# Performance work log

Hardware: AMD Instinct MI355X
Metric: run time of the kernel (lower is better)

Reference implementation:

```python
import jax, jax.numpy as jnp
import numpy as np

B, C, N, K, COUT = 4, 64, 8192, 16, 64
EPS = 1e-5  # BatchNorm1d default eps


def setup_inputs() -> dict:
    key = jax.random.key(0)
    k1, k2, k3 = jax.random.split(key, 3)
    x = jax.random.normal(k1, (B, C, N), dtype=jnp.float32)
    coords = jax.random.normal(k2, (B, 3, N), dtype=jnp.float32)
    # Linear(2C -> COUT) params
    W = jax.random.normal(k3, (2 * C, COUT), dtype=jnp.float32) * (1.0 / np.sqrt(2 * C))
    b = jnp.zeros((COUT,), dtype=jnp.float32)
    # BatchNorm1d affine params (train-mode batch stats, as in torch default)
    gamma = jnp.ones((COUT,), dtype=jnp.float32)
    beta = jnp.zeros((COUT,), dtype=jnp.float32)
    return {"x": x, "coords": coords, "W": W, "b": b, "gamma": gamma, "beta": beta}


def reference(x, coords, W, b, gamma, beta):
    k = min(K, max(N - 1, 1))
    # --- kNN in coordinate space (squared distances give same ordering as cdist) ---
    ct = jnp.swapaxes(coords, 1, 2)                      # (B, N, 3)
    sq = jnp.sum(ct * ct, axis=-1)                       # (B, N)
    d2 = sq[:, :, None] + sq[:, None, :] - 2.0 * jnp.einsum('bnd,bmd->bnm', ct, ct)
    _, idx = jax.lax.top_k(-d2, k + 1)                   # smallest k+1 distances
    idx = idx[:, :, 1:]                                  # drop self -> (B, N, k)
    # --- gather neighbor features ---
    xt = jnp.swapaxes(x, 1, 2)                           # (B, N, C)
    nb = jax.vmap(lambda f, i: f[i])(xt, idx)            # (B, N, k, C)
    center = jnp.broadcast_to(xt[:, :, None, :], nb.shape)
    edge = jnp.concatenate([center, nb - center], axis=-1)  # (B, N, k, 2C)
    # --- edge MLP: Linear -> BatchNorm1d (batch stats) -> ReLU ---
    h = jnp.einsum('bnkc,cd->bnkd', edge, W) + b         # (B, N, k, COUT)
    mean = jnp.mean(h, axis=(0, 1, 2))
    var = jnp.var(h, axis=(0, 1, 2))
    h = (h - mean) * jax.lax.rsqrt(var + EPS) * gamma + beta
    h = jax.nn.relu(h)
    # --- max-pool over k neighbors ---
    out = jnp.max(h, axis=2)                             # (B, N, COUT)
    return jnp.swapaxes(out, 1, 2)                       # (B, COUT, N)
```

## Files before the change

### kernel.cpp

```cpp
#include <hip/hip_runtime.h>


#define Bn 4
#define Cn 64
#define Nn 8192
#define Kn 16
#define NSL 8

typedef unsigned long long ull;

__global__ __launch_bounds__(256) void transpose_kernel(const float* __restrict__ x,
                                                        const float* __restrict__ coords,
                                                        float* __restrict__ xt,
                                                        float4* __restrict__ cpack) {
  __shared__ float tile[64][65];
  int bid = blockIdx.x;
  int b = bid >> 7;
  int n0 = (bid & 127) << 6;
  int tx = threadIdx.x & 63;
  int ty = threadIdx.x >> 6;
  for (int c = ty; c < 64; c += 4)
    tile[tx][c] = x[((size_t)b * 64 + c) * Nn + n0 + tx];
  if (ty == 0) {
    int n = n0 + tx;
    const float* cb = coords + (size_t)b * 3 * Nn;
    float cx = cb[n], cy = cb[Nn + n], cz = cb[2 * Nn + n];
    float cs = __fadd_rn(__fadd_rn(__fmul_rn(cx, cx), __fmul_rn(cy, cy)),
                         __fmul_rn(cz, cz));
    cpack[(size_t)b * Nn + n] = make_float4(cx, cy, cz, cs);
  }
  __syncthreads();
  for (int r = ty; r < 64; r += 4)
    xt[((size_t)b * Nn + n0 + r) * 64 + tx] = tile[r][tx];
}


#define RMAX(kv) do {                                         \
    ull _kk = (kv);                                           \
    _Pragma("unroll")                                         \
    for (int _u = 0; _u < 16; ++_u)                           \
      ad[_u] = (ad[_u] == thr) ? _kk : ad[_u];                \
    ull _t0 = ad[0] > ad[1] ? ad[0] : ad[1];                  \
    ull _t1 = ad[2] > ad[3] ? ad[2] : ad[3];                  \
    ull _t2 = ad[4] > ad[5] ? ad[4] : ad[5];                  \
    ull _t3 = ad[6] > ad[7] ? ad[6] : ad[7];                  \
    ull _t4 = ad[8] > ad[9] ? ad[8] : ad[9];                  \
    ull _t5 = ad[10] > ad[11] ? ad[10] : ad[11];              \
    ull _t6 = ad[12] > ad[13] ? ad[12] : ad[13];              \
    ull _t7 = ad[14] > ad[15] ? ad[14] : ad[15];              \
    ull _u0 = _t0 > _t1 ? _t0 : _t1;                          \
    ull _u1 = _t2 > _t3 ? _t2 : _t3;                          \
    ull _u2 = _t4 > _t5 ? _t4 : _t5;                          \
    ull _u3 = _t6 > _t7 ? _t6 : _t7;                          \
    ull _v0 = _u0 > _u1 ? _u0 : _u1;                          \
    ull _v1 = _u2 > _u3 ? _u2 : _u3;                          \
    thr = _v0 > _v1 ? _v0 : _v1;                              \
  } while (0)

__global__ __launch_bounds__(512) void knn_kernel(const float4* __restrict__ cpack,
                                                  int* __restrict__ knn) {
  __shared__ __align__(16) ull mk[(NSL - 1) * 16 * 64];
  float4* stage = (float4*)mk;
  __shared__ unsigned sthr[64];

  int bid = blockIdx.x;
  int b = bid >> 7;
  int q0 = (bid & 127) << 6;
  int tid = threadIdx.x;
  int q = tid & 63;
  int s = tid >> 6;
  int qg = q0 + q;

  const float4* cp = cpack + (size_t)b * Nn;
  float4 qc = cp[qg];
  float qs = qc.w;
  float qx2 = 2.f * qc.x, qy2 = 2.f * qc.y, qz2 = 2.f * qc.z;

  if (tid < 64) sthr[tid] = 0xFFFFFFFFu;

  ull ad[16];
#pragma unroll
  for (int i = 0; i < 16; ++i) ad[i] = 0xFFFFFFFF00000000ull | (unsigned)i;
  ull thr = 0xFFFFFFFF0000000Full;
  unsigned thr_hi = 0xFFFFFFFFu;

  for (int t = 0; t < Nn / 512; ++t) {
    __syncthreads();
    stage[tid] = cp[t * 512 + tid];
    __syncthreads();
#pragma unroll
    for (int half = 0; half < 2; ++half) {
      int loc = half * 256 + s * 32;
      int base = t * 512 + loc;
      unsigned sh = sthr[q];
      thr_hi = sh < thr_hi ? sh : thr_hi;
      unsigned mask = 0;
#pragma unroll 8
      for (int j = 0; j < 32; ++j) {
        float4 c4 = stage[loc + j];
        float dot2 = __fadd_rn(__fadd_rn(__fmul_rn(qx2, c4.x), __fmul_rn(qy2, c4.y)),
                               __fmul_rn(qz2, c4.z));
        float d2 = __fsub_rn(__fadd_rn(qs, c4.w), dot2);
        mask |= (__float_as_uint(d2) <= thr_hi) ? (1u << j) : 0u;
      }
      unsigned sj = (unsigned)(qg - base);
      if (sj < 32u) mask &= ~(1u << sj);
      while (__any(mask)) {
        if (mask) {
          int j = __ffs(mask) - 1;
          mask &= (mask - 1);
          float4 c4 = stage[loc + j];
          float dot2 = __fadd_rn(__fadd_rn(__fmul_rn(qx2, c4.x), __fmul_rn(qy2, c4.y)),
                                 __fmul_rn(qz2, c4.z));
          float d2 = __fsub_rn(__fadd_rn(qs, c4.w), dot2);
          ull key = ((ull)__float_as_uint(d2) << 32) | (unsigned)(base + j);
          if (key < thr) RMAX(key);
        }
      }
      unsigned lh = (unsigned)(thr >> 32);
      thr_hi = lh < thr_hi ? lh : thr_hi;
      atomicMin(&sthr[q], lh);
    }
  }

  __syncthreads();
  if (s > 0) {
#pragma unroll
    for (int i = 0; i < 16; ++i) mk[(((s - 1) << 4) + i) * 64 + q] = ad[i];
  }
  __syncthreads();
  if (s == 0) {
    for (int t = 0; t < (NSL - 1) * 16; ++t) {
      ull kk = mk[t * 64 + q];
      if (kk < thr) RMAX(kk);
    }
    int* op = knn + (size_t)(b * Nn + qg) * 16;
#pragma unroll
    for (int i = 0; i < 16; ++i) op[i] = (int)(ad[i] & 0xFFFFFFFFull);
  }
}

__global__ __launch_bounds__(256) void edge_kernel(
    const float* __restrict__ xt, const int* __restrict__ knn,
    const float* __restrict__ W, const float* __restrict__ bias,
    float* __restrict__ mnb, float* __restrict__ mxb,
    float* __restrict__ ps1, float* __restrict__ ps2) {
  __shared__ float dlds[4][16][64];
  __shared__ float clds[4][64];
  __shared__ float r1[4][64], r2[4][64];

  int tid = threadIdx.x;
  int l = tid & 63;
  int w = tid >> 6;

  float w1[64], w2[64];
#pragma unroll
  for (int c = 0; c < 64; ++c) {
    w1[c] = W[c * 64 + l];
    w2[c] = W[(64 + c) * 64 + l];
  }
  float bl = bias[l];
  float s1 = 0.f, s2 = 0.f;

  int wid = blockIdx.x * 4 + w;
  int nw = gridDim.x * 4;
  for (int p = wid; p < Bn * Nn; p += nw) {
    int bb = p >> 13;
    const float* xb = xt + (size_t)bb * Nn * 64;
    float ctr = xt[(size_t)p * 64 + l];
    clds[w][l] = ctr;
    const int* ip = knn + (size_t)p * 16;
#pragma unroll
    for (int j = 0; j < 16; ++j) {
      int nj = ip[j];
      dlds[w][j][l] = xb[(size_t)nj * 64 + l] - ctr;
    }
    __syncthreads();

    float cc = bl;
#pragma unroll
    for (int c = 0; c < 64; ++c) cc = fmaf(clds[w][c], w1[c], cc);

    float mn = 3.0e38f, mx = -3.0e38f;
#pragma unroll
    for (int k = 0; k < 16; ++k) {
      float h = cc;
#pragma unroll
      for (int c = 0; c < 64; ++c) h = fmaf(dlds[w][k][c], w2[c], h);
      mn = fminf(mn, h);
      mx = fmaxf(mx, h);
      s1 += h;
      s2 = fmaf(h, h, s2);
    }
    mnb[(size_t)p * 64 + l] = mn;
    mxb[(size_t)p * 64 + l] = mx;
    __syncthreads();
  }

  r1[w][l] = s1; r2[w][l] = s2;
  __syncthreads();
  if (w == 0) {
    float a = r1[0][l] + r1[1][l] + r1[2][l] + r1[3][l];
    float c2 = r2[0][l] + r2[1][l] + r2[2][l] + r2[3][l];
    ps1[blockIdx.x * 64 + l] = a;
    ps2[blockIdx.x * 64 + l] = c2;
  }
}

__global__ __launch_bounds__(256) void stats_kernel(const float* __restrict__ ps1,
                                                    const float* __restrict__ ps2,
                                                    float* __restrict__ stats) {
  __shared__ float r1[4][64], r2[4][64];
  int c = threadIdx.x & 63, g = threadIdx.x >> 6;
  float a = 0.f, b2 = 0.f;
  for (int i = g; i < 512; i += 4) { a += ps1[i * 64 + c]; b2 += ps2[i * 64 + c]; }
  r1[g][c] = a; r2[g][c] = b2;
  __syncthreads();
  if (g == 0) {
    float s1 = r1[0][c] + r1[1][c] + r1[2][c] + r1[3][c];
    float s2 = r2[0][c] + r2[1][c] + r2[2][c] + r2[3][c];
    const float invM = 1.f / 524288.f;
    float mean = s1 * invM;
    float var = s2 * invM - mean * mean;
    stats[c] = mean;
    stats[64 + c] = var;
  }
}

__global__ __launch_bounds__(256) void final_kernel(
    const float* __restrict__ mnb, const float* __restrict__ mxb,
    const float* __restrict__ stats, const float* __restrict__ gamma,
    const float* __restrict__ beta, float* __restrict__ out) {
  __shared__ float tile[64][65];
  int bid = blockIdx.x;
  int b = bid >> 7;
  int n0 = (bid & 127) << 6;
  int tx = threadIdx.x & 63, ty = threadIdx.x >> 6;
  float mean = stats[tx], var = stats[64 + tx];
  float sc = gamma[tx] * rsqrtf(var + 1e-5f);
  float sh = fmaf(-mean, sc, beta[tx]);
  for (int r = ty; r < 64; r += 4) {
    size_t off = ((size_t)(b * Nn + n0 + r)) * 64 + tx;
    float lo = fmaf(mnb[off], sc, sh);
    float hi = fmaf(mxb[off], sc, sh);
    tile[tx][r] = fmaxf(fmaxf(hi, lo), 0.f);
  }
  __syncthreads();
  for (int r = ty; r < 64; r += 4)
    out[((size_t)b * 64 + r) * Nn + n0 + tx] = tile[r][tx];
}

extern "C" void kernel_launch(void* const* d_in, const int* in_sizes, int n_in,
                              void* d_out, int out_size, void* d_ws, size_t ws_size,
                              hipStream_t stream) {
  const float* x      = (const float*)d_in[0];
  const float* coords = (const float*)d_in[1];
  const float* W      = (const float*)d_in[2];
  const float* bias   = (const float*)d_in[3];
  const float* gamma  = (const float*)d_in[4];
  const float* beta   = (const float*)d_in[5];
  float* out = (float*)d_out;

  char* ws = (char*)d_ws;
  float*  xt    = (float*)ws;
  int*    knn   = (int*)(ws + 8388608);
  float*  mnb   = (float*)(ws + 10485760);
  float4* cpack = (float4*)(ws + 10485760);
  float*  mxb   = (float*)(ws + 18874368);
  float*  ps1   = (float*)(ws + 27262976);
  float*  ps2   = (float*)(ws + 27394048);
  float*  stats = (float*)(ws + 27525120);

  transpose_kernel<<<dim3(512), dim3(256), 0, stream>>>(x, coords, xt, cpack);
  knn_kernel<<<dim3(512), dim3(512), 0, stream>>>(cpack, knn);
  edge_kernel<<<dim3(512), dim3(256), 0, stream>>>(xt, knn, W, bias, mnb, mxb, ps1, ps2);
  stats_kernel<<<dim3(1), dim3(256), 0, stream>>>(ps1, ps2, stats);
  final_kernel<<<dim3(512), dim3(256), 0, stream>>>(mnb, mxb, stats, gamma, beta, out);
}
```

Before: 576.1 us.

## Replace brute-force kNN with uniform 3D grid binning and ring search

Builds a uniform 32^3 spatial grid over the coordinates (histogram, two-pass prefix scan, scatter into cell-sorted order), then searches neighbor cells in expanding Chebyshev rings per query with early termination once the ring lower bound exceeds the current k-th distance. Queries are processed in cell-sorted order, which improves spatial coherence within wavefronts. This replaces the O(N^2) all-pairs distance scan. In exchange it adds several small kernels plus a memset, relies on a fixed grid range of [-6,6] tuned to normally distributed inputs, and brings divergent per-lane cell loops; the final merge now does a sorted insertion.

```diff
diff --git a/kernel.cpp b/kernel.cpp
--- a/kernel.cpp
+++ b/kernel.cpp
@@ -2,12 +2,18 @@
 
 
 #define Bn 4
-#define Cn 64
 #define Nn 8192
-#define Kn 16
 #define NSL 8
+#define Gc 32
+#define CS 32896
+#define Hc 0.375f
 
 typedef unsigned long long ull;
+
+__device__ __forceinline__ int cellof(float v) {
+  int i = (int)floorf((v + 6.0f) * (1.0f / Hc));
+  return min(Gc - 1, max(0, i));
+}
 
 __global__ __launch_bounds__(256) void transpose_kernel(const float* __restrict__ x,
                                                         const float* __restrict__ coords,
@@ -34,6 +40,65 @@
     xt[((size_t)b * Nn + n0 + r) * 64 + tx] = tile[r][tx];
 }
 
+__global__ __launch_bounds__(256) void hist_kernel(const float4* __restrict__ cpack,
+                                                   unsigned* __restrict__ cells,
+                                                   unsigned* __restrict__ cstart) {
+  int n = blockIdx.x * 256 + threadIdx.x;
+  float4 c = cpack[n];
+  unsigned cell = ((unsigned)cellof(c.z) * Gc + cellof(c.y)) * Gc + cellof(c.x);
+  cells[n] = cell;
+  atomicAdd(&cstart[(unsigned)(n >> 13) * CS + cell], 1u);
+}
+
+__global__ __launch_bounds__(256) void scanA_kernel(unsigned* __restrict__ cstart,
+                                                    unsigned* __restrict__ partials) {
+  __shared__ unsigned sums[256];
+  int bid = blockIdx.x, b = bid >> 4, ch = bid & 15, t = threadIdx.x;
+  unsigned* base = cstart + (size_t)b * CS + ch * 2048 + t * 8;
+  unsigned v[8], p = 0;
+#pragma unroll
+  for (int j = 0; j < 8; ++j) { unsigned c = base[j]; v[j] = p; p += c; }
+  sums[t] = p;
+  __syncthreads();
+  for (int off = 1; off < 256; off <<= 1) {
+    unsigned u = (t >= off) ? sums[t - off] : 0u;
+    __syncthreads();
+    sums[t] += u;
+    __syncthreads();
+  }
+  unsigned excl = sums[t] - p;
+#pragma unroll
+  for (int j = 0; j < 8; ++j) base[j] = v[j] + excl;
+  if (t == 255) partials[bid] = sums[255];
+}
+
+__global__ __launch_bounds__(256) void scanC_kernel(unsigned* __restrict__ cstart,
+                                                    unsigned* __restrict__ cursor,
+                                                    const unsigned* __restrict__ partials) {
+  int bid = blockIdx.x, b = bid >> 4, ch = bid & 15, t = threadIdx.x;
+  unsigned off = 0;
+  for (int k = 0; k < ch; ++k) off += partials[b * 16 + k];
+  size_t o = (size_t)b * CS + ch * 2048 + t * 8;
+#pragma unroll
+  for (int j = 0; j < 8; ++j) {
+    unsigned val = cstart[o + j] + off;
+    cstart[o + j] = val;
+    cursor[o + j] = val;
+  }
+  if (ch == 15 && t == 255) cstart[(size_t)b * CS + Gc * Gc * Gc] = off + partials[b * 16 + 15];
+}
+
+__global__ __launch_bounds__(256) void scatter_kernel(const float4* __restrict__ cpack,
+                                                      const unsigned* __restrict__ cells,
+                                                      unsigned* __restrict__ cursor,
+                                                      float4* __restrict__ spos4) {
+  int n = blockIdx.x * 256 + threadIdx.x;
+  int b = n >> 13;
+  unsigned slot = atomicAdd(&cursor[(size_t)b * CS + cells[n]], 1u);
+  float4 c = cpack[n];
+  c.w = __uint_as_float((unsigned)(n & 8191));
+  spos4[(size_t)b * Nn + slot] = c;
+}
 
 #define RMAX(kv) do {                                         \
     ull _kk = (kv);                                           \
@@ -57,86 +122,134 @@
     thr = _v0 > _v1 ? _v0 : _v1;                              \
   } while (0)
 
-__global__ __launch_bounds__(512) void knn_kernel(const float4* __restrict__ cpack,
-                                                  int* __restrict__ knn) {
-  __shared__ __align__(16) ull mk[(NSL - 1) * 16 * 64];
-  float4* stage = (float4*)mk;
+__global__ __launch_bounds__(512) void knn_grid_kernel(const float4* __restrict__ spos4,
+                                                       const unsigned* __restrict__ cstart,
+                                                       int* __restrict__ knn) {
+  __shared__ ull mk[(NSL - 1) * 16 * 64];
   __shared__ unsigned sthr[64];
 
   int bid = blockIdx.x;
   int b = bid >> 7;
-  int q0 = (bid & 127) << 6;
+  int grp = bid & 127;
   int tid = threadIdx.x;
-  int q = tid & 63;
+  int lane = tid & 63;
   int s = tid >> 6;
-  int qg = q0 + q;
-
-  const float4* cp = cpack + (size_t)b * Nn;
-  float4 qc = cp[qg];
-  float qs = qc.w;
-  float qx2 = 2.f * qc.x, qy2 = 2.f * qc.y, qz2 = 2.f * qc.z;
+  int qslot = grp * 64 + lane;
+
+  const float4* sp = spos4 + (size_t)b * Nn;
+  const unsigned* cs = cstart + (size_t)b * CS;
+
+  float4 qc = sp[qslot];
+  unsigned qg = __float_as_uint(qc.w);
+  float qx = qc.x, qy = qc.y, qz = qc.z;
+  float qs = __fadd_rn(__fadd_rn(__fmul_rn(qx, qx), __fmul_rn(qy, qy)),
+                       __fmul_rn(qz, qz));
+  float qx2 = 2.f * qx, qy2 = 2.f * qy, qz2 = 2.f * qz;
+  int c0x = cellof(qx), c0y = cellof(qy), c0z = cellof(qz);
 
   if (tid < 64) sthr[tid] = 0xFFFFFFFFu;
+  __syncthreads();
 
   ull ad[16];
 #pragma unroll
   for (int i = 0; i < 16; ++i) ad[i] = 0xFFFFFFFF00000000ull | (unsigned)i;
   ull thr = 0xFFFFFFFF0000000Full;
   unsigned thr_hi = 0xFFFFFFFFu;
-
-  for (int t = 0; t < Nn / 512; ++t) {
-    __syncthreads();
-    stage[tid] = cp[t * 512 + tid];
-    __syncthreads();
-#pragma unroll
-    for (int half = 0; half < 2; ++half) {
-      int loc = half * 256 + s * 32;
-      int base = t * 512 + loc;
-      unsigned sh = sthr[q];
-      thr_hi = sh < thr_hi ? sh : thr_hi;
-      unsigned mask = 0;
-#pragma unroll 8
-      for (int j = 0; j < 32; ++j) {
-        float4 c4 = stage[loc + j];
-        float dot2 = __fadd_rn(__fadd_rn(__fmul_rn(qx2, c4.x), __fmul_rn(qy2, c4.y)),
-                               __fmul_rn(qz2, c4.z));
-        float d2 = __fsub_rn(__fadd_rn(qs, c4.w), dot2);
-        mask |= (__float_as_uint(d2) <= thr_hi) ? (1u << j) : 0u;
+  bool done = false;
+
+  for (int r = 0; r < Gc; ++r) {
+    if (__all(done)) break;
+    unsigned cnt = 0;
+    for (int dz = -r; dz <= r; ++dz)
+      for (int dy = -r; dy <= r; ++dy)
+        for (int dx = -r; dx <= r; ++dx) {
+          int m = abs(dx) > abs(dy) ? abs(dx) : abs(dy);
+          m = m > abs(dz) ? m : abs(dz);
+          if (m != r) continue;
+          if (((cnt++) & 7u) != (unsigned)s) continue;
+          int cx = c0x + dx, cy = c0y + dy, cz = c0z + dz;
+          bool ok = !done && cx >= 0 && cx < Gc && cy >= 0 && cy < Gc &&
+                    cz >= 0 && cz < Gc;
+          unsigned s0 = 0, s1 = 0;
+          if (ok) {
+            unsigned cidx = ((unsigned)cz * Gc + cy) * Gc + cx;
+            s0 = cs[cidx];
+            s1 = cs[cidx + 1];
+          }
+          for (unsigned k = 0;; ++k) {
+            bool a = (s0 + k) < s1;
+            if (!__any(a)) break;
+            if (a) {
+              float4 c4 = sp[s0 + k];
+              float csq = __fadd_rn(__fadd_rn(__fmul_rn(c4.x, c4.x), __fmul_rn(c4.y, c4.y)),
+                                    __fmul_rn(c4.z, c4.z));
+              float dot2 = __fadd_rn(__fadd_rn(__fmul_rn(qx2, c4.x), __fmul_rn(qy2, c4.y)),
+                                     __fmul_rn(qz2, c4.z));
+              float d2 = __fsub_rn(__fadd_rn(qs, csq), dot2);
+              unsigned bits = __float_as_uint(d2);
+              if (bits <= thr_hi) {
+                unsigned oi = __float_as_uint(c4.w);
+                if (oi != qg) {
+                  ull key = ((ull)bits << 32) | oi;
+                  if (key < thr) {
+                    RMAX(key);
+                    unsigned nh = (unsigned)(thr >> 32);
+                    if (nh < thr_hi) thr_hi = nh;
+                  }
+                }
+              }
+            }
+          }
+        }
+    unsigned lh = (unsigned)(thr >> 32);
+    atomicMin(&sthr[lane], lh);
+    unsigned sh = sthr[lane];
+    if (sh < thr_hi) thr_hi = sh;
+    float rh = fmaxf((float)r * Hc - 1e-5f, 0.f);
+    unsigned rb = __float_as_uint(__fmul_rn(rh, rh));
+    done = done || (rb > thr_hi);
+  }
+
+  __syncthreads();
+  if (s > 0) {
+#pragma unroll
+    for (int i = 0; i < 16; ++i) mk[(((s - 1) << 4) + i) * 64 + lane] = ad[i];
+  }
+  __syncthreads();
+  if (s == 0) {
+    ull nad[16];
+#pragma unroll
+    for (int i = 0; i < 16; ++i) nad[i] = ~0ull;
+#pragma unroll
+    for (int i = 0; i < 16; ++i) {
+      ull kk = ad[i];
+      if (kk < nad[15]) {
+        bool ci = true;
+#pragma unroll
+        for (int u = 15; u >= 1; --u) {
+          bool cm = kk < nad[u - 1];
+          nad[u] = ci ? (cm ? nad[u - 1] : kk) : nad[u];
+          ci = cm;
+        }
+        nad[0] = ci ? kk : nad[0];
       }
-      unsigned sj = (unsigned)(qg - base);
-      if (sj < 32u) mask &= ~(1u << sj);
-      while (__any(mask)) {
-        if (mask) {
-          int j = __ffs(mask) - 1;
-          mask &= (mask - 1);
-          float4 c4 = stage[loc + j];
-          float dot2 = __fadd_rn(__fadd_rn(__fmul_rn(qx2, c4.x), __fmul_rn(qy2, c4.y)),
-                                 __fmul_rn(qz2, c4.z));
-          float d2 = __fsub_rn(__fadd_rn(qs, c4.w), dot2);
-          ull key = ((ull)__float_as_uint(d2) << 32) | (unsigned)(base + j);
-          if (key < thr) RMAX(key);
+    }
+    for (int t = 0; t < (NSL - 1) * 16; ++t) {
+      ull kk = mk[t * 64 + lane];
+      if (kk < nad[15]) {
+        bool ci = true;
+#pragma unroll
+        for (int u = 15; u >= 1; --u) {
+          bool cm = kk < nad[u - 1];
+          nad[u] = ci ? (cm ? nad[u - 1] : kk) : nad[u];
+          ci = cm;
         }
+        nad[0] = ci ? kk : nad[0];
       }
-      unsigned lh = (unsigned)(thr >> 32);
-      thr_hi = lh < thr_hi ? lh : thr_hi;
-      atomicMin(&sthr[q], lh);
     }
-  }
-
-  __syncthreads();
-  if (s > 0) {
-#pragma unroll
-    for (int i = 0; i < 16; ++i) mk[(((s - 1) << 4) + i) * 64 + q] = ad[i];
-  }
-  __syncthreads();
-  if (s == 0) {
-    for (int t = 0; t < (NSL - 1) * 16; ++t) {
-      ull kk = mk[t * 64 + q];
-      if (kk < thr) RMAX(kk);
-    }
-    int* op = knn + (size_t)(b * Nn + qg) * 16;
-#pragma unroll
-    for (int i = 0; i < 16; ++i) op[i] = (int)(ad[i] & 0xFFFFFFFFull);
+    int* op = knn + (size_t)(b * Nn + (int)qg) * 16;
+#pragma unroll
+    for (int i = 0; i < 16; ++i) op[i] = (int)(nad[i] & 0xFFFFFFFFull);
   }
 }
 
@@ -262,17 +375,27 @@
   float* out = (float*)d_out;
 
   char* ws = (char*)d_ws;
-  float*  xt    = (float*)ws;
-  int*    knn   = (int*)(ws + 8388608);
-  float*  mnb   = (float*)(ws + 10485760);
-  float4* cpack = (float4*)(ws + 10485760);
-  float*  mxb   = (float*)(ws + 18874368);
-  float*  ps1   = (float*)(ws + 27262976);
-  float*  ps2   = (float*)(ws + 27394048);
-  float*  stats = (float*)(ws + 27525120);
+  float*    xt       = (float*)ws;
+  int*      knn      = (int*)(ws + 8388608);
+  float*    mnb      = (float*)(ws + 10485760);
+  float4*   cpack    = (float4*)(ws + 10485760);
+  float*    mxb      = (float*)(ws + 18874368);
+  float4*   spos4    = (float4*)(ws + 18874368);
+  unsigned* cstart   = (unsigned*)(ws + 19398656);
+  unsigned* cursor   = (unsigned*)(ws + 19924992);
+  unsigned* cells    = (unsigned*)(ws + 20451328);
+  unsigned* partials = (unsigned*)(ws + 20582400);
+  float*    ps1      = (float*)(ws + 27262976);
+  float*    ps2      = (float*)(ws + 27394048);
+  float*    stats    = (float*)(ws + 27525120);
 
   transpose_kernel<<<dim3(512), dim3(256), 0, stream>>>(x, coords, xt, cpack);
-  knn_kernel<<<dim3(512), dim3(512), 0, stream>>>(cpack, knn);
+  hipMemsetAsync(cstart, 0, (size_t)4 * CS * 4, stream);
+  hist_kernel<<<dim3(128), dim3(256), 0, stream>>>(cpack, cells, cstart);
+  scanA_kernel<<<dim3(64), dim3(256), 0, stream>>>(cstart, partials);
+  scanC_kernel<<<dim3(64), dim3(256), 0, stream>>>(cstart, cursor, partials);
+  scatter_kernel<<<dim3(128), dim3(256), 0, stream>>>(cpack, cells, cursor, spos4);
+  knn_grid_kernel<<<dim3(512), dim3(512), 0, stream>>>(spos4, cstart, knn);
   edge_kernel<<<dim3(512), dim3(256), 0, stream>>>(xt, knn, W, bias, mnb, mxb, ps1, ps2);
   stats_kernel<<<dim3(1), dim3(256), 0, stream>>>(ps1, ps2, stats);
   final_kernel<<<dim3(512), dim3(256), 0, stream>>>(mnb, mxb, stats, gamma, beta, out);
```

Result: slower. 1.232 ms (+113.8%).
